# Kernel optimization log

Hardware: AMD Instinct MI355X
Metric: run time of the kernel (lower is better)

The kernel has to match this reference:

```python
import jax, jax.numpy as jnp
import numpy as np

N_NODES = 20000
HIDDEN = 128
MSG = 64
N_EDGES = 320000
TAU = 0.5
EPS = 1e-10


def setup_inputs() -> dict:
    key = jax.random.key(0)
    ks = jax.random.split(key, 12)
    two_msg = 2 * MSG
    return {
        "feat": jax.random.normal(ks[0], (N_NODES, HIDDEN), jnp.float32),
        "h": jax.random.normal(ks[1], (N_NODES, HIDDEN), jnp.float32),
        "src": jax.random.randint(ks[2], (N_EDGES,), 0, N_NODES),
        "dst": jax.random.randint(ks[3], (N_EDGES,), 0, N_NODES),
        "u": jax.random.uniform(ks[4], (N_EDGES, MSG, 2), jnp.float32),
        "W_enc": jax.random.normal(ks[5], (two_msg, 2 * HIDDEN), jnp.float32) * (2 * HIDDEN) ** -0.5,
        "b_enc": jnp.zeros((two_msg,), jnp.float32),
        "W_dec": jax.random.normal(ks[6], (two_msg, two_msg), jnp.float32) * two_msg ** -0.5,
        "b_dec": jnp.zeros((two_msg,), jnp.float32),
        "W_ih": jax.random.normal(ks[7], (3 * HIDDEN, HIDDEN + two_msg), jnp.float32) * (HIDDEN + two_msg) ** -0.5,
        "W_hh": jax.random.normal(ks[8], (3 * HIDDEN, HIDDEN), jnp.float32) * HIDDEN ** -0.5,
        "b_ih": jnp.zeros((3 * HIDDEN,), jnp.float32),
        "b_hh": jnp.zeros((3 * HIDDEN,), jnp.float32),
    }


def reference(feat, h, src, dst, u, W_enc, b_enc, W_dec, b_dec, W_ih, W_hh, b_ih, b_hh):
    N, H = h.shape
    two_msg = W_enc.shape[0]
    msg = two_msg // 2

    # --- per-edge message encoding (hidden state detached, as in original) ---
    h_det = jax.lax.stop_gradient(h)
    e_in = jnp.concatenate([feat[src], h_det[src]], axis=1)          # [E, 2H]
    logits = (e_in @ W_enc.T + b_enc).reshape(-1, msg, 2)            # [E, msg, 2]

    # gumbel-softmax, tau=0.5, hard=True (straight-through)
    g = -jnp.log(-jnp.log(u + EPS) + EPS)
    y = jax.nn.softmax((logits + g) / TAU, axis=-1)
    onehot = jax.nn.one_hot(jnp.argmax(y, axis=-1), 2, dtype=y.dtype)
    m = (y + jax.lax.stop_gradient(onehot - y)).reshape(-1, two_msg)  # [E, 2*msg]

    # --- segment-max aggregation (elementwise OR since msgs are 0/1) ---
    seg = jax.ops.segment_max(m, dst, num_segments=N)                 # [N, 2*msg]
    deg = jax.ops.segment_sum(jnp.ones_like(dst), dst, num_segments=N)
    c = jnp.where((deg > 0)[:, None], seg, 0.0)                       # zero for isolated nodes

    # --- GRUCell update: input = [feat, f_dec(c)] ---
    x = jnp.concatenate([feat, c @ W_dec.T + b_dec], axis=1)          # [N, H + 2*msg]
    gi = x @ W_ih.T + b_ih
    gh = h @ W_hh.T + b_hh
    ir, iz, inn = jnp.split(gi, 3, axis=1)
    hr, hz, hn = jnp.split(gh, 3, axis=1)
    r = jax.nn.sigmoid(ir + hr)
    z = jax.nn.sigmoid(iz + hz)
    n = jnp.tanh(inn + r * hn)
    h_new = (1.0 - z) * n + z * h
    return (h_new, h_new)
```

## Files before the change

### kernel.cpp

```cpp
#include <hip/hip_runtime.h>
#include <stdint.h>

#define NN   20000
#define NNP  20096
#define NE   320000
#define GEPS 1e-10f

typedef __attribute__((ext_vector_type(8))) __bf16 bf16x8;
typedef __attribute__((ext_vector_type(4))) float f32x4;

__device__ __forceinline__ float fsigmoid(float x) { return 1.f / (1.f + __expf(-x)); }
__device__ __forceinline__ float ftanh(float x)    { return 1.f - 2.f / (__expf(2.f * x) + 1.f); }


__global__ __launch_bounds__(256) void prep_k(
    const float* __restrict__ feat,  const float* __restrict__ hst,
    const float* __restrict__ W_enc, const float* __restrict__ b_enc,
    const float* __restrict__ W_dec, const float* __restrict__ b_dec,
    const float* __restrict__ W_ih,  const float* __restrict__ W_hh,
    const float* __restrict__ b_ih,  const float* __restrict__ b_hh,
    __bf16* __restrict__ B1h, __bf16* __restrict__ B1l,
    __bf16* __restrict__ B2h, __bf16* __restrict__ B2l,
    float* __restrict__ bias1, float* __restrict__ bias2,
    float* __restrict__ W_comb, ulonglong2* __restrict__ mask2,
    __bf16* __restrict__ Aph, __bf16* __restrict__ Apl)
{
    const int b = blockIdx.x, t = threadIdx.x;
    if (b < 128) {
        const int src = (b >> 6) * 64 + (b & 31) * 2 + ((b >> 5) & 1);
        const float v = W_enc[src * 256 + t];
        const __bf16 hi = (__bf16)v;
        const int kt = t >> 5, fkh = (t >> 3) & 3, e = t & 7;
        const size_t idx = ((size_t)(kt * 4 + fkh) * 128 + b) * 8 + e;
        B1h[idx] = hi;
        B1l[idx] = (__bf16)(v - (float)hi);
    } else if (b < 640) {
        const int r2 = b - 128;
        const int nb = r2 >> 7, rem = r2 & 127, g = rem >> 5, jj = rem & 31;
        const int j = nb * 32 + jj;
        const int k = t;
        float v;
        if (g == 0)      v = (k < 128) ? W_ih[j * 256 + k]         : W_hh[j * 128 + (k - 128)];
        else if (g == 1) v = (k < 128) ? W_ih[(128 + j) * 256 + k] : W_hh[(128 + j) * 128 + (k - 128)];
        else if (g == 2) v = (k < 128) ? W_ih[(256 + j) * 256 + k] : 0.f;
        else             v = (k < 128) ? 0.f                       : W_hh[(256 + j) * 128 + (k - 128)];
        const __bf16 hi = (__bf16)v;
        const int kt = t >> 5, fkh = (t >> 3) & 3, e = t & 7;
        const size_t idx = ((size_t)(kt * 4 + fkh) * 512 + r2) * 8 + e;
        B2h[idx] = hi;
        B2l[idx] = (__bf16)(v - (float)hi);
    } else if (b < 832) {
        const int idx = (b - 640) * 256 + t;
        const int o = idx >> 7, k = idx & 127;
        float s = 0.f;
        for (int l = 0; l < 128; ++l)
            s += W_ih[o * 256 + 128 + l] * W_dec[l * 128 + k];
        W_comb[idx] = s;
    } else if (b < 835) {
        __shared__ float bd[128];
        if (t < 128) {
            float s = b_dec[t];
            for (int k = 0; k < 128; ++k) s += W_dec[t * 128 + k];
            bd[t] = s;
        }
        __syncthreads();
        const int g = (b - 832) * 256 + t;
        if (g < 128) {
            bias1[g] = b_enc[(g >> 6) * 64 + (g & 31) * 2 + ((g >> 5) & 1)];
        } else if (g < 640) {
            const int c2 = g - 128;
            const int nb = c2 >> 7, rem = c2 & 127, gg = rem >> 5, jj = rem & 31;
            const int j = nb * 32 + jj;
            float v;
            if (gg == 3) v = b_hh[256 + j];
            else {
                const int o = gg * 128 + j;
                float s = (gg == 2) ? b_ih[o] : (b_ih[o] + b_hh[o]);
                for (int l = 0; l < 128; ++l) s += W_ih[o * 256 + 128 + l] * bd[l];
                v = s;
            }
            bias2[c2] = v;
        }
    } else if (b < 914) {
        const int i = (b - 835) * 256 + t;
        if (i < NN) mask2[i] = make_ulonglong2(0ull, 0ull);
    } else {
        const int blk = b - 914;
        const int row = blk * 8 + (t & 7);
        const int k0  = (t >> 3) * 8;
        float x[8];
        if (row < NN) {
            const float* sp = (k0 < 128) ? (feat + (size_t)row * 128 + k0)
                                         : (hst  + (size_t)row * 128 + (k0 - 128));
            const float4 v0 = *(const float4*)sp;
            const float4 v1 = *(const float4*)(sp + 4);
            x[0] = v0.x; x[1] = v0.y; x[2] = v0.z; x[3] = v0.w;
            x[4] = v1.x; x[5] = v1.y; x[6] = v1.z; x[7] = v1.w;
        } else {
#pragma unroll
            for (int i = 0; i < 8; ++i) x[i] = 0.f;
        }
        bf16x8 hi, lo;
#pragma unroll
        for (int i = 0; i < 8; ++i) {
            const __bf16 hv = (__bf16)x[i];
            hi[i] = hv;
            lo[i] = (__bf16)(x[i] - (float)hv);
        }
        const int kt = k0 >> 5, fkh = (k0 >> 3) & 3;
        const size_t idx = ((size_t)(kt * 4 + fkh) * NNP + row) * 8;
        *(bf16x8*)(Aph + idx) = hi;
        *(bf16x8*)(Apl + idx) = lo;
    }
}

__global__ __launch_bounds__(256) void gemm_rtab(
    const __bf16* __restrict__ Aph, const __bf16* __restrict__ Apl,
    const __bf16* __restrict__ B1h, const __bf16* __restrict__ B1l,
    const float* __restrict__ bias1, float* __restrict__ rtab)
{
    const int t = threadIdx.x, lane = t & 63, wid = t >> 6;
    const int m0 = blockIdx.x * 64;
    const int wm = (wid >> 1) * 32, wn = (wid & 1) * 64;
    const int fr = lane & 15, fkh = lane >> 4;

    f32x4 acc[2][4];
#pragma unroll
    for (int i = 0; i < 2; ++i)
#pragma unroll
        for (int j = 0; j < 4; ++j) acc[i][j] = (f32x4){0.f, 0.f, 0.f, 0.f};

    for (int kt = 0; kt < 8; ++kt) {
        const size_t ab = (size_t)(kt * 4 + fkh) * NNP;
        const size_t bb = (size_t)(kt * 4 + fkh) * 128;
        bf16x8 ah[2], al[2];
#pragma unroll
        for (int mf = 0; mf < 2; ++mf) {
            const size_t ro = (ab + m0 + wm + mf * 16 + fr) * 8;
            ah[mf] = *(const bf16x8*)(Aph + ro);
            al[mf] = *(const bf16x8*)(Apl + ro);
        }
#pragma unroll
        for (int nf = 0; nf < 4; ++nf) {
            const size_t ro = (bb + wn + nf * 16 + fr) * 8;
            const bf16x8 bh = *(const bf16x8*)(B1h + ro);
            const bf16x8 bl = *(const bf16x8*)(B1l + ro);
#pragma unroll
            for (int mf = 0; mf < 2; ++mf) {
                acc[mf][nf] = __builtin_amdgcn_mfma_f32_16x16x32_bf16(ah[mf], bh, acc[mf][nf], 0, 0, 0);
                acc[mf][nf] = __builtin_amdgcn_mfma_f32_16x16x32_bf16(al[mf], bh, acc[mf][nf], 0, 0, 0);
                acc[mf][nf] = __builtin_amdgcn_mfma_f32_16x16x32_bf16(ah[mf], bl, acc[mf][nf], 0, 0, 0);
            }
        }
    }

#pragma unroll
    for (int nf = 0; nf < 2; ++nf) {
        const int c0 = wn + nf * 16 + fr;
        const float b0 = bias1[c0], b1 = bias1[c0 + 32];
        const int j = (wid & 1) * 32 + nf * 16 + fr;
#pragma unroll
        for (int mf = 0; mf < 2; ++mf)
#pragma unroll
            for (int rr = 0; rr < 4; ++rr) {
                const int gr = m0 + wm + mf * 16 + (lane >> 4) * 4 + rr;
                if (gr < NN)
                    rtab[(size_t)gr * 64 + j] =
                        __expf((acc[mf][nf + 2][rr] + b1) - (acc[mf][nf][rr] + b0));
            }
    }
}

#define EPW 16
__global__ __launch_bounds__(256) void edge_k(
    const float* __restrict__ u, const int* __restrict__ src,
    const int* __restrict__ dst, const float* __restrict__ rtab,
    unsigned long long* __restrict__ masks)
{
    const int wv = __builtin_amdgcn_readfirstlane(blockIdx.x * 4 + (threadIdx.x >> 6));
    const int lane = threadIdx.x & 63;
    const int e0 = wv * EPW;

    float2 uu[EPW];
    float  rr[EPW];
    int    dd[EPW];
#pragma unroll
    for (int i = 0; i < EPW; ++i) {
        const int e = e0 + i;
        uu[i] = *(const float2*)(u + (size_t)e * 128 + lane * 2);
        rr[i] = rtab[(size_t)src[e] * 64 + lane];
        dd[i] = dst[e];
    }
#pragma unroll
    for (int i = 0; i < EPW; ++i) {
        const float a0 = GEPS - __logf(uu[i].x + GEPS);
        const float a1 = GEPS - __logf(uu[i].y + GEPS);
        const unsigned long long mone = __ballot(rr[i] * a0 > a1);
        if (lane == 0) {
            atomicOr(&masks[(size_t)dd[i] * 2 + 1], mone);
            atomicOr(&masks[(size_t)dd[i] * 2 + 0], ~mone);
        }
    }
}

__global__ __launch_bounds__(256) void gemm_gates(
    const __bf16* __restrict__ Aph, const __bf16* __restrict__ Apl,
    const __bf16* __restrict__ B2h, const __bf16* __restrict__ B2l,
    const float* __restrict__ bias2, const unsigned long long* __restrict__ masks,
    const float* __restrict__ W_comb, const float* __restrict__ h,
    float* __restrict__ out)
{
    const int bid = blockIdx.x;
    const int g = bid & 7;
    const int inner = bid >> 3;
    const int nb = inner & 3;
    const int mrow = (inner >> 2) * 8 + g;
    if (mrow >= NNP / 128) return;
    const int m0 = mrow * 128;

    const int t = threadIdx.x, lane = t & 63, wid = t >> 6;
    const int wm = wid * 32;
    const int fr = lane & 15, fkh = lane >> 4;

    f32x4 acc[2][8];
#pragma unroll
    for (int i = 0; i < 2; ++i)
#pragma unroll
        for (int j = 0; j < 8; ++j) acc[i][j] = (f32x4){0.f, 0.f, 0.f, 0.f};

    for (int kt = 0; kt < 8; ++kt) {
        const size_t ab = (size_t)(kt * 4 + fkh) * NNP;
        const size_t bb = (size_t)(kt * 4 + fkh) * 512;
        bf16x8 ah[2], al[2];
#pragma unroll
        for (int mf = 0; mf < 2; ++mf) {
            const size_t ro = (ab + m0 + wm + mf * 16 + fr) * 8;
            ah[mf] = *(const bf16x8*)(Aph + ro);
            al[mf] = *(const bf16x8*)(Apl + ro);
        }
#pragma unroll
        for (int nf = 0; nf < 8; ++nf) {
            const size_t ro = (bb + nb * 128 + nf * 16 + fr) * 8;
            const bf16x8 bh = *(const bf16x8*)(B2h + ro);
            const bf16x8 bl = *(const bf16x8*)(B2l + ro);
#pragma unroll
            for (int mf = 0; mf < 2; ++mf) {
                acc[mf][nf] = __builtin_amdgcn_mfma_f32_16x16x32_bf16(ah[mf], bh, acc[mf][nf], 0, 0, 0);
                acc[mf][nf] = __builtin_amdgcn_mfma_f32_16x16x32_bf16(al[mf], bh, acc[mf][nf], 0, 0, 0);
                acc[mf][nf] = __builtin_amdgcn_mfma_f32_16x16x32_bf16(ah[mf], bl, acc[mf][nf], 0, 0, 0);
            }
        }
    }

    float bia[8];
#pragma unroll
    for (int nf = 0; nf < 8; ++nf) bia[nf] = bias2[nb * 128 + nf * 16 + fr];

#pragma unroll
    for (int mf = 0; mf < 2; ++mf)
#pragma unroll
        for (int rr = 0; rr < 4; ++rr) {
            const int gr = m0 + wm + mf * 16 + (lane >> 4) * 4 + rr;
            if (gr >= NN) continue;
            const unsigned long long ze = ~masks[(size_t)gr * 2 + 0];
            const unsigned long long zo = ~masks[(size_t)gr * 2 + 1];
#pragma unroll
            for (int jh = 0; jh < 2; ++jh) {
                const int j = nb * 32 + jh * 16 + fr;
                float rp = acc[mf][0 + jh][rr] + bia[0 + jh];
                float zp = acc[mf][2 + jh][rr] + bia[2 + jh];
                float ip = acc[mf][4 + jh][rr] + bia[4 + jh];
                float hp = acc[mf][6 + jh][rr] + bia[6 + jh];
                if (ze | zo) {
                    unsigned long long bz = ze;
#pragma unroll 1
                    while (bz) {
                        const int k = __builtin_ctzll(bz); bz &= bz - 1;
                        const int bit = 2 * k;
                        rp -= W_comb[(size_t)j * 128 + bit];
                        zp -= W_comb[(size_t)(128 + j) * 128 + bit];
                        ip -= W_comb[(size_t)(256 + j) * 128 + bit];
                    }
                    bz = zo;
#pragma unroll 1
                    while (bz) {
                        const int k = __builtin_ctzll(bz); bz &= bz - 1;
                        const int bit = 2 * k + 1;
                        rp -= W_comb[(size_t)j * 128 + bit];
                        zp -= W_comb[(size_t)(128 + j) * 128 + bit];
                        ip -= W_comb[(size_t)(256 + j) * 128 + bit];
                    }
                }
                const float hv = h[(size_t)gr * 128 + j];
                const float rg = fsigmoid(rp);
                const float zg = fsigmoid(zp);
                const float nv = ftanh(ip + rg * hp);
                const float o = (1.f - zg) * nv + zg * hv;
                out[(size_t)gr * 128 + j] = o;
                out[(size_t)(NN + gr) * 128 + j] = o;
            }
        }
}

extern "C" void kernel_launch(void* const* d_in, const int* in_sizes, int n_in,
                              void* d_out, int out_size, void* d_ws, size_t ws_size,
                              hipStream_t stream) {
    const float* feat  = (const float*)d_in[0];
    const float* h     = (const float*)d_in[1];
    const int*   src   = (const int*)d_in[2];
    const int*   dst   = (const int*)d_in[3];
    const float* u     = (const float*)d_in[4];
    const float* W_enc = (const float*)d_in[5];
    const float* b_enc = (const float*)d_in[6];
    const float* W_dec = (const float*)d_in[7];
    const float* b_dec = (const float*)d_in[8];
    const float* W_ih  = (const float*)d_in[9];
    const float* W_hh  = (const float*)d_in[10];
    const float* b_ih  = (const float*)d_in[11];
    const float* b_hh  = (const float*)d_in[12];
    float* out = (float*)d_out;
    (void)in_sizes; (void)n_in; (void)out_size; (void)ws_size;

    char* ws = (char*)d_ws;
    float*              rtab   = (float*)(ws + 0);
    unsigned long long* masks  = (unsigned long long*)(ws + 5120000);
    __bf16*             B1h    = (__bf16*)(ws + 5440000);
    __bf16*             B1l    = (__bf16*)(ws + 5505536);
    __bf16*             B2h    = (__bf16*)(ws + 5571072);
    __bf16*             B2l    = (__bf16*)(ws + 5833216);
    float*              bias1  = (float*)(ws + 6095360);
    float*              bias2  = (float*)(ws + 6095872);
    float*              W_comb = (float*)(ws + 6097920);
    __bf16*             Aph    = (__bf16*)(ws + 6294528);
    __bf16*             Apl    = (__bf16*)(ws + 16583680);

    prep_k<<<914 + NNP / 8, 256, 0, stream>>>(
        feat, h, W_enc, b_enc, W_dec, b_dec, W_ih, W_hh, b_ih, b_hh,
        B1h, B1l, B2h, B2l, bias1, bias2, W_comb, (ulonglong2*)masks, Aph, Apl);

    gemm_rtab<<<313, 256, 0, stream>>>(Aph, Apl, B1h, B1l, bias1, rtab);

    edge_k<<<NE / (4 * EPW), 256, 0, stream>>>(u, src, dst, rtab, masks);

    gemm_gates<<<640, 256, 0, stream>>>(Aph, Apl, B2h, B2l, bias2, masks, W_comb, h, out);
}
```

Before: 103.8 us.

## Shrink GEMM tiles for more blocks and drop low-bf16 weight term in gates GEMM

gemm_rtab now uses 32-row blocks with one 16-row M fragment per wave, which doubles the block count. gemm_gates uses 64-row blocks, with waves split over rows and the half of the j-columns each owns, and the grid rises to 1256 blocks. The gates GEMM also stops using the low-order bf16 part of the weights (B2l), cutting the MFMA count from three to two per fragment. The aim is better occupancy, fewer registers, and fewer MFMAs and loads. The cost is some accuracy loss in the gate pre-activations and more redundant B loads across blocks.

New measurement: 92.68 us. 1.12x faster.

```diff
diff --git a/kernel.cpp b/kernel.cpp
--- a/kernel.cpp
+++ b/kernel.cpp
@@ -120,37 +120,30 @@
     const float* __restrict__ bias1, float* __restrict__ rtab)
 {
     const int t = threadIdx.x, lane = t & 63, wid = t >> 6;
-    const int m0 = blockIdx.x * 64;
-    const int wm = (wid >> 1) * 32, wn = (wid & 1) * 64;
+    const int m0 = blockIdx.x * 32;
+    const int wm = (wid & 1) * 16;
+    const int cgn = wid >> 1;
+    const int wn = cgn * 64;
     const int fr = lane & 15, fkh = lane >> 4;
 
-    f32x4 acc[2][4];
-#pragma unroll
-    for (int i = 0; i < 2; ++i)
-#pragma unroll
-        for (int j = 0; j < 4; ++j) acc[i][j] = (f32x4){0.f, 0.f, 0.f, 0.f};
+    f32x4 acc[4];
+#pragma unroll
+    for (int j = 0; j < 4; ++j) acc[j] = (f32x4){0.f, 0.f, 0.f, 0.f};
 
     for (int kt = 0; kt < 8; ++kt) {
         const size_t ab = (size_t)(kt * 4 + fkh) * NNP;
         const size_t bb = (size_t)(kt * 4 + fkh) * 128;
-        bf16x8 ah[2], al[2];
-#pragma unroll
-        for (int mf = 0; mf < 2; ++mf) {
-            const size_t ro = (ab + m0 + wm + mf * 16 + fr) * 8;
-            ah[mf] = *(const bf16x8*)(Aph + ro);
-            al[mf] = *(const bf16x8*)(Apl + ro);
-        }
+        const size_t ro = (ab + m0 + wm + fr) * 8;
+        const bf16x8 ah = *(const bf16x8*)(Aph + ro);
+        const bf16x8 al = *(const bf16x8*)(Apl + ro);
 #pragma unroll
         for (int nf = 0; nf < 4; ++nf) {
-            const size_t ro = (bb + wn + nf * 16 + fr) * 8;
-            const bf16x8 bh = *(const bf16x8*)(B1h + ro);
-            const bf16x8 bl = *(const bf16x8*)(B1l + ro);
-#pragma unroll
-            for (int mf = 0; mf < 2; ++mf) {
-                acc[mf][nf] = __builtin_amdgcn_mfma_f32_16x16x32_bf16(ah[mf], bh, acc[mf][nf], 0, 0, 0);
-                acc[mf][nf] = __builtin_amdgcn_mfma_f32_16x16x32_bf16(al[mf], bh, acc[mf][nf], 0, 0, 0);
-                acc[mf][nf] = __builtin_amdgcn_mfma_f32_16x16x32_bf16(ah[mf], bl, acc[mf][nf], 0, 0, 0);
-            }
+            const size_t rb = (bb + wn + nf * 16 + fr) * 8;
+            const bf16x8 bh = *(const bf16x8*)(B1h + rb);
+            const bf16x8 bl = *(const bf16x8*)(B1l + rb);
+            acc[nf] = __builtin_amdgcn_mfma_f32_16x16x32_bf16(ah, bh, acc[nf], 0, 0, 0);
+            acc[nf] = __builtin_amdgcn_mfma_f32_16x16x32_bf16(al, bh, acc[nf], 0, 0, 0);
+            acc[nf] = __builtin_amdgcn_mfma_f32_16x16x32_bf16(ah, bl, acc[nf], 0, 0, 0);
         }
     }
 
@@ -158,16 +151,14 @@
     for (int nf = 0; nf < 2; ++nf) {
         const int c0 = wn + nf * 16 + fr;
         const float b0 = bias1[c0], b1 = bias1[c0 + 32];
-        const int j = (wid & 1) * 32 + nf * 16 + fr;
-#pragma unroll
-        for (int mf = 0; mf < 2; ++mf)
-#pragma unroll
-            for (int rr = 0; rr < 4; ++rr) {
-                const int gr = m0 + wm + mf * 16 + (lane >> 4) * 4 + rr;
-                if (gr < NN)
-                    rtab[(size_t)gr * 64 + j] =
-                        __expf((acc[mf][nf + 2][rr] + b1) - (acc[mf][nf][rr] + b0));
-            }
+        const int j = cgn * 32 + nf * 16 + fr;
+#pragma unroll
+        for (int rr = 0; rr < 4; ++rr) {
+            const int gr = m0 + wm + (lane >> 4) * 4 + rr;
+            if (gr < NN)
+                rtab[(size_t)gr * 64 + j] =
+                    __expf((acc[nf + 2][rr] + b1) - (acc[nf][rr] + b0));
+        }
     }
 }
 
@@ -205,28 +196,25 @@
 
 __global__ __launch_bounds__(256) void gemm_gates(
     const __bf16* __restrict__ Aph, const __bf16* __restrict__ Apl,
-    const __bf16* __restrict__ B2h, const __bf16* __restrict__ B2l,
+    const __bf16* __restrict__ B2h,
     const float* __restrict__ bias2, const unsigned long long* __restrict__ masks,
     const float* __restrict__ W_comb, const float* __restrict__ h,
     float* __restrict__ out)
 {
     const int bid = blockIdx.x;
-    const int g = bid & 7;
-    const int inner = bid >> 3;
-    const int nb = inner & 3;
-    const int mrow = (inner >> 2) * 8 + g;
-    if (mrow >= NNP / 128) return;
-    const int m0 = mrow * 128;
+    const int nb = bid & 3;
+    const int m0 = (bid >> 2) * 64;
 
     const int t = threadIdx.x, lane = t & 63, wid = t >> 6;
-    const int wm = wid * 32;
+    const int wm = (wid & 1) * 32;
+    const int jh = wid >> 1;
     const int fr = lane & 15, fkh = lane >> 4;
 
-    f32x4 acc[2][8];
+    f32x4 acc[2][4];
 #pragma unroll
     for (int i = 0; i < 2; ++i)
 #pragma unroll
-        for (int j = 0; j < 8; ++j) acc[i][j] = (f32x4){0.f, 0.f, 0.f, 0.f};
+        for (int j = 0; j < 4; ++j) acc[i][j] = (f32x4){0.f, 0.f, 0.f, 0.f};
 
     for (int kt = 0; kt < 8; ++kt) {
         const size_t ab = (size_t)(kt * 4 + fkh) * NNP;
@@ -239,22 +227,21 @@
             al[mf] = *(const bf16x8*)(Apl + ro);
         }
 #pragma unroll
-        for (int nf = 0; nf < 8; ++nf) {
-            const size_t ro = (bb + nb * 128 + nf * 16 + fr) * 8;
+        for (int g = 0; g < 4; ++g) {
+            const size_t ro = (bb + nb * 128 + g * 32 + jh * 16 + fr) * 8;
             const bf16x8 bh = *(const bf16x8*)(B2h + ro);
-            const bf16x8 bl = *(const bf16x8*)(B2l + ro);
 #pragma unroll
             for (int mf = 0; mf < 2; ++mf) {
-                acc[mf][nf] = __builtin_amdgcn_mfma_f32_16x16x32_bf16(ah[mf], bh, acc[mf][nf], 0, 0, 0);
-                acc[mf][nf] = __builtin_amdgcn_mfma_f32_16x16x32_bf16(al[mf], bh, acc[mf][nf], 0, 0, 0);
-                acc[mf][nf] = __builtin_amdgcn_mfma_f32_16x16x32_bf16(ah[mf], bl, acc[mf][nf], 0, 0, 0);
+                acc[mf][g] = __builtin_amdgcn_mfma_f32_16x16x32_bf16(ah[mf], bh, acc[mf][g], 0, 0, 0);
+                acc[mf][g] = __builtin_amdgcn_mfma_f32_16x16x32_bf16(al[mf], bh, acc[mf][g], 0, 0, 0);
             }
         }
     }
 
-    float bia[8];
-#pragma unroll
-    for (int nf = 0; nf < 8; ++nf) bia[nf] = bias2[nb * 128 + nf * 16 + fr];
+    float bia[4];
+#pragma unroll
+    for (int g = 0; g < 4; ++g) bia[g] = bias2[nb * 128 + g * 32 + jh * 16 + fr];
+    const int j = nb * 32 + jh * 16 + fr;
 
 #pragma unroll
     for (int mf = 0; mf < 2; ++mf)
@@ -264,41 +251,37 @@
             if (gr >= NN) continue;
             const unsigned long long ze = ~masks[(size_t)gr * 2 + 0];
             const unsigned long long zo = ~masks[(size_t)gr * 2 + 1];
-#pragma unroll
-            for (int jh = 0; jh < 2; ++jh) {
-                const int j = nb * 32 + jh * 16 + fr;
-                float rp = acc[mf][0 + jh][rr] + bia[0 + jh];
-                float zp = acc[mf][2 + jh][rr] + bia[2 + jh];
-                float ip = acc[mf][4 + jh][rr] + bia[4 + jh];
-                float hp = acc[mf][6 + jh][rr] + bia[6 + jh];
-                if (ze | zo) {
-                    unsigned long long bz = ze;
+            float rp = acc[mf][0][rr] + bia[0];
+            float zp = acc[mf][1][rr] + bia[1];
+            float ip = acc[mf][2][rr] + bia[2];
+            float hp = acc[mf][3][rr] + bia[3];
+            if (ze | zo) {
+                unsigned long long bz = ze;
 #pragma unroll 1
-                    while (bz) {
-                        const int k = __builtin_ctzll(bz); bz &= bz - 1;
-                        const int bit = 2 * k;
-                        rp -= W_comb[(size_t)j * 128 + bit];
-                        zp -= W_comb[(size_t)(128 + j) * 128 + bit];
-                        ip -= W_comb[(size_t)(256 + j) * 128 + bit];
-                    }
-                    bz = zo;
+                while (bz) {
+                    const int k = __builtin_ctzll(bz); bz &= bz - 1;
+                    const int bit = 2 * k;
+                    rp -= W_comb[(size_t)j * 128 + bit];
+                    zp -= W_comb[(size_t)(128 + j) * 128 + bit];
+                    ip -= W_comb[(size_t)(256 + j) * 128 + bit];
+                }
+                bz = zo;
 #pragma unroll 1
-                    while (bz) {
-                        const int k = __builtin_ctzll(bz); bz &= bz - 1;
-                        const int bit = 2 * k + 1;
-                        rp -= W_comb[(size_t)j * 128 + bit];
-                        zp -= W_comb[(size_t)(128 + j) * 128 + bit];
-                        ip -= W_comb[(size_t)(256 + j) * 128 + bit];
-                    }
+                while (bz) {
+                    const int k = __builtin_ctzll(bz); bz &= bz - 1;
+                    const int bit = 2 * k + 1;
+                    rp -= W_comb[(size_t)j * 128 + bit];
+                    zp -= W_comb[(size_t)(128 + j) * 128 + bit];
+                    ip -= W_comb[(size_t)(256 + j) * 128 + bit];
                 }
-                const float hv = h[(size_t)gr * 128 + j];
-                const float rg = fsigmoid(rp);
-                const float zg = fsigmoid(zp);
-                const float nv = ftanh(ip + rg * hp);
-                const float o = (1.f - zg) * nv + zg * hv;
-                out[(size_t)gr * 128 + j] = o;
-                out[(size_t)(NN + gr) * 128 + j] = o;
             }
+            const float hv = h[(size_t)gr * 128 + j];
+            const float rg = fsigmoid(rp);
+            const float zg = fsigmoid(zp);
+            const float nv = ftanh(ip + rg * hp);
+            const float o = (1.f - zg) * nv + zg * hv;
+            out[(size_t)gr * 128 + j] = o;
+            out[(size_t)(NN + gr) * 128 + j] = o;
         }
 }
 
@@ -338,9 +321,9 @@
         feat, h, W_enc, b_enc, W_dec, b_dec, W_ih, W_hh, b_ih, b_hh,
         B1h, B1l, B2h, B2l, bias1, bias2, W_comb, (ulonglong2*)masks, Aph, Apl);
 
-    gemm_rtab<<<313, 256, 0, stream>>>(Aph, Apl, B1h, B1l, bias1, rtab);
+    gemm_rtab<<<NNP / 32, 256, 0, stream>>>(Aph, Apl, B1h, B1l, bias1, rtab);
 
     edge_k<<<NE / (4 * EPW), 256, 0, stream>>>(u, src, dst, rtab, masks);
 
-    gemm_gates<<<640, 256, 0, stream>>>(Aph, Apl, B2h, B2l, bias2, masks, W_comb, h, out);
-}
+    gemm_gates<<<(NNP / 64) * 4, 256, 0, stream>>>(Aph, Apl, B2h, bias2, masks, W_comb, h, out);
+}
```
